# Performance work log

Measured on AMD Instinct MI355X. Metric: run time of the kernel, lower is better.

The kernel has to match this reference:

```python
import jax, jax.numpy as jnp
import numpy as np

N, E, H, C, HC = 16384, 262144, 4, 128, 512
G, IN, ED, OUT, NCLS = 8, 5, 2, 256, 12
EPS = 1e-5


def _gatv2(x, src, dst, ea, Wl, Wr, We, att, b):
    # GATv2Conv (PyG): score = att . leaky_relu(lin_l(x_j) + lin_r(x_i) + lin_e(e))
    xl = (x @ Wl).reshape(-1, H, C)          # source transform [N,H,C]
    xr = (x @ Wr).reshape(-1, H, C)          # target transform [N,H,C]
    ee = (ea @ We).reshape(-1, H, C)         # edge embedding   [E,H,C]
    s = jax.nn.leaky_relu(xl[src] + xr[dst] + ee, 0.2)
    logit = jnp.einsum('ehc,hc->eh', s, att)            # [E,H]
    m = jax.ops.segment_max(logit, dst, num_segments=N)  # per-dst max
    a = jnp.exp(logit - m[dst])
    denom = jax.ops.segment_sum(a, dst, num_segments=N)
    alpha = a / (denom[dst] + 1e-16)                     # segment softmax
    out = jax.ops.segment_sum(xl[src] * alpha[:, :, None], dst, num_segments=N)
    return out.reshape(-1, HC) + b


def _bn(x, g, b):  # BatchNorm1d, training-mode batch stats
    mu = x.mean(0)
    var = x.var(0)
    return g * (x - mu) * jax.lax.rsqrt(var + EPS) + b


def setup_inputs() -> dict:
    key = jax.random.key(0)
    ks = iter(jax.random.split(key, 32))
    d = {}
    d['x'] = jax.random.normal(next(ks), (N, IN), jnp.float32)
    d['edge_attr'] = jax.random.normal(next(ks), (E, ED), jnp.float32)
    d['edge_index'] = jax.random.randint(next(ks), (2, E), 0, N)
    d['batch'] = jnp.sort(jax.random.randint(next(ks), (N,), 0, G))
    for i, din in zip((1, 2, 3), (IN, HC, HC)):
        d[f'c{i}_Wl'] = jax.random.normal(next(ks), (din, HC), jnp.float32) * 0.05
        d[f'c{i}_Wr'] = jax.random.normal(next(ks), (din, HC), jnp.float32) * 0.05
        d[f'c{i}_We'] = jax.random.normal(next(ks), (ED, HC), jnp.float32) * 0.05
        d[f'c{i}_att'] = jax.random.normal(next(ks), (H, C), jnp.float32) * 0.05
        d[f'c{i}_b'] = jnp.zeros((HC,), jnp.float32)
        d[f'bn{i}_g'] = jnp.ones((HC,), jnp.float32)
        d[f'bn{i}_b'] = jnp.zeros((HC,), jnp.float32)
    d['ge_W1'] = jax.random.normal(next(ks), (HC, OUT), jnp.float32) * 0.05
    d['ge_b1'] = jnp.zeros((OUT,), jnp.float32)
    d['ge_W2'] = jax.random.normal(next(ks), (OUT, OUT), jnp.float32) * 0.05
    d['ge_b2'] = jnp.zeros((OUT,), jnp.float32)
    d['cls_W'] = jax.random.normal(next(ks), (OUT, NCLS), jnp.float32) * 0.05
    d['cls_b'] = jnp.zeros((NCLS,), jnp.float32)
    return d


def reference(x, edge_attr, edge_index, batch,
              c1_Wl, c1_Wr, c1_We, c1_att, c1_b, bn1_g, bn1_b,
              c2_Wl, c2_Wr, c2_We, c2_att, c2_b, bn2_g, bn2_b,
              c3_Wl, c3_Wr, c3_We, c3_att, c3_b, bn3_g, bn3_b,
              ge_W1, ge_b1, ge_W2, ge_b2, cls_W, cls_b):
    src, dst = edge_index[0], edge_index[1]
    x1 = jax.nn.elu(_bn(_gatv2(x, src, dst, edge_attr, c1_Wl, c1_Wr, c1_We, c1_att, c1_b), bn1_g, bn1_b))
    x2 = jax.nn.elu(_bn(_gatv2(x1, src, dst, edge_attr, c2_Wl, c2_Wr, c2_We, c2_att, c2_b), bn2_g, bn2_b)) + x1
    x3 = jax.nn.elu(_bn(_gatv2(x2, src, dst, edge_attr, c3_Wl, c3_Wr, c3_We, c3_att, c3_b), bn3_g, bn3_b)) + x2
    cnt = jax.ops.segment_sum(jnp.ones((N,), x3.dtype), batch, num_segments=G)
    x_pool = jax.ops.segment_sum(x3, batch, num_segments=G) / cnt[:, None]
    emb = jax.nn.relu(x_pool @ ge_W1 + ge_b1) @ ge_W2 + ge_b2
    logits = emb @ cls_W + cls_b
    return logits, emb
```

## Files before the change

### kernel.cpp

```cpp
#include <hip/hip_runtime.h>
#include <math.h>

#define NN    16384
#define NE    262144
#define NHEAD 4
#define HC    512
#define NG    8

typedef __bf16 bf16x8 __attribute__((ext_vector_type(8)));
typedef float floatx4 __attribute__((ext_vector_type(4)));
typedef float f32x2 __attribute__((ext_vector_type(2)));

__device__ __forceinline__ f32x2 sp2(float s) { return (f32x2){s, s}; }
__device__ __forceinline__ f32x2 pkmax(f32x2 a, f32x2 b) {
    f32x2 r; r.x = fmaxf(a.x, b.x); r.y = fmaxf(a.y, b.y); return r;
}

__device__ __forceinline__ unsigned short f2bf(float f) {
    union { float f; unsigned u; } v{f};
    unsigned r = v.u + 0x7FFFu + ((v.u >> 16) & 1u);
    return (unsigned short)(r >> 16);
}
__device__ __forceinline__ float bf2f(unsigned short b) {
    return __uint_as_float((unsigned)b << 16);
}

__device__ __forceinline__ void unpk8v(uint4 v, f32x2* f) {
    f[0] = (f32x2){__uint_as_float(v.x << 16), __uint_as_float(v.x & 0xFFFF0000u)};
    f[1] = (f32x2){__uint_as_float(v.y << 16), __uint_as_float(v.y & 0xFFFF0000u)};
    f[2] = (f32x2){__uint_as_float(v.z << 16), __uint_as_float(v.z & 0xFFFF0000u)};
    f[3] = (f32x2){__uint_as_float(v.w << 16), __uint_as_float(v.w & 0xFFFF0000u)};
}

#define GLD16(g, l) __builtin_amdgcn_global_load_lds( \
    (const __attribute__((address_space(1))) void*)(g), \
    (__attribute__((address_space(3))) void*)(l), 16, 0, 0)

__global__ void k_hist(const int* __restrict__ dst, int* __restrict__ cnt) {
    int e = blockIdx.x * 256 + threadIdx.x;
    if (e < NE) atomicAdd(&cnt[dst[e]], 1);
}

__global__ __launch_bounds__(1024) void k_scan(const int* __restrict__ cnt,
                                               int* __restrict__ rp,
                                               int* __restrict__ offp,
                                               const int* __restrict__ batch,
                                               int* __restrict__ gcnt) {
    __shared__ int part[1024];
    int t = threadIdx.x;
    if (t < NG) {
        int lb[2];
#pragma unroll
        for (int q = 0; q < 2; q++) {
            int target = t + q;
            int lo = 0, hi = NN;
            while (lo < hi) {
                int mid = (lo + hi) >> 1;
                if (batch[mid] < target) lo = mid + 1; else hi = mid;
            }
            lb[q] = lo;
        }
        gcnt[t] = lb[1] - lb[0];
    }
    int base = t * 16;
    int loc[16];
    int s = 0;
#pragma unroll
    for (int i = 0; i < 16; i++) { loc[i] = s; s += cnt[base + i]; }
    part[t] = s;
    __syncthreads();
    for (int off = 1; off < 1024; off <<= 1) {
        int v = 0;
        if (t >= off) v = part[t - off];
        __syncthreads();
        if (t >= off) part[t] += v;
        __syncthreads();
    }
    int excl = (t == 0) ? 0 : part[t - 1];
#pragma unroll
    for (int i = 0; i < 16; i++) {
        int r = excl + loc[i];
        rp[base + i] = r;
        offp[base + i] = r;
    }
    if (t == 1023) rp[NN] = excl + s;
}

__global__ void k_fill(const int* __restrict__ dst, const int* __restrict__ src,
                       const float* __restrict__ ea, int* __restrict__ offp,
                       int* __restrict__ csrc, float2* __restrict__ ce) {
    int e = blockIdx.x * 256 + threadIdx.x;
    if (e < NE) {
        int d = dst[e];
        int pos = atomicAdd(&offp[d], 1);
        csrc[pos] = src[e];
        ce[pos] = *(const float2*)(ea + 2 * (size_t)e);
    }
}

__global__ __launch_bounds__(256) void k_lin1(const float* __restrict__ x,
                                              const float* __restrict__ Wl,
                                              const float* __restrict__ Wr,
                                              unsigned short* __restrict__ xl,
                                              unsigned short* __restrict__ xr) {
    int n = blockIdx.x * 4 + (threadIdx.x >> 6);
    int lane = threadIdx.x & 63;
    int j0 = lane << 3;
    float xs[5];
#pragma unroll
    for (int k = 0; k < 5; k++) xs[k] = x[n * 5 + k];
    float al[8] = {}, ar[8] = {};
#pragma unroll
    for (int k = 0; k < 5; k++) {
        float4 wl0 = *(const float4*)(Wl + k * 512 + j0);
        float4 wl1 = *(const float4*)(Wl + k * 512 + j0 + 4);
        float4 wr0 = *(const float4*)(Wr + k * 512 + j0);
        float4 wr1 = *(const float4*)(Wr + k * 512 + j0 + 4);
        al[0] += xs[k] * wl0.x; al[1] += xs[k] * wl0.y; al[2] += xs[k] * wl0.z; al[3] += xs[k] * wl0.w;
        al[4] += xs[k] * wl1.x; al[5] += xs[k] * wl1.y; al[6] += xs[k] * wl1.z; al[7] += xs[k] * wl1.w;
        ar[0] += xs[k] * wr0.x; ar[1] += xs[k] * wr0.y; ar[2] += xs[k] * wr0.z; ar[3] += xs[k] * wr0.w;
        ar[4] += xs[k] * wr1.x; ar[5] += xs[k] * wr1.y; ar[6] += xs[k] * wr1.z; ar[7] += xs[k] * wr1.w;
    }
    ushort4 o0, o1;
    o0.x = f2bf(al[0]); o0.y = f2bf(al[1]); o0.z = f2bf(al[2]); o0.w = f2bf(al[3]);
    o1.x = f2bf(al[4]); o1.y = f2bf(al[5]); o1.z = f2bf(al[6]); o1.w = f2bf(al[7]);
    *(ushort4*)(xl + (size_t)n * 512 + j0) = o0;
    *(ushort4*)(xl + (size_t)n * 512 + j0 + 4) = o1;
    o0.x = f2bf(ar[0]); o0.y = f2bf(ar[1]); o0.z = f2bf(ar[2]); o0.w = f2bf(ar[3]);
    o1.x = f2bf(ar[4]); o1.y = f2bf(ar[5]); o1.z = f2bf(ar[6]); o1.w = f2bf(ar[7]);
    *(ushort4*)(xr + (size_t)n * 512 + j0) = o0;
    *(ushort4*)(xr + (size_t)n * 512 + j0 + 4) = o1;
}

__global__ __launch_bounds__(256) void k_wt4(const float* __restrict__ W0,
                                             const float* __restrict__ W1,
                                             const float* __restrict__ W2,
                                             const float* __restrict__ W3,
                                             unsigned short* __restrict__ Wt2,
                                             unsigned short* __restrict__ Wt3) {
    __shared__ float tile[64][65];
    int bid = blockIdx.x;
    int mat = bid >> 6, sub = bid & 63;
    const float* W = (mat == 0) ? W0 : (mat == 1) ? W1 : (mat == 2) ? W2 : W3;
    unsigned short* Wt = (mat == 0) ? Wt2 : (mat == 1) ? (Wt2 + 512 * 512)
                       : (mat == 2) ? Wt3 : (Wt3 + 512 * 512);
    int n0 = (sub & 7) * 64, k0 = (sub >> 3) * 64;
    int lr = threadIdx.x >> 4;
    int lc = (threadIdx.x & 15) << 2;
    for (int r = lr; r < 64; r += 16) {
        float4 v = *(const float4*)(W + (size_t)(k0 + r) * 512 + n0 + lc);
        tile[r][lc] = v.x; tile[r][lc + 1] = v.y; tile[r][lc + 2] = v.z; tile[r][lc + 3] = v.w;
    }
    __syncthreads();
    for (int r = lr; r < 64; r += 16) {
        ushort4 o;
        o.x = f2bf(tile[lc + 0][r]); o.y = f2bf(tile[lc + 1][r]);
        o.z = f2bf(tile[lc + 2][r]); o.w = f2bf(tile[lc + 3][r]);
        *(ushort4*)(Wt + (size_t)(n0 + r) * 512 + k0 + lc) = o;
    }
}

#define BM 128
#define BN 128
#define BK 64

__global__ __launch_bounds__(256) void k_gemm_bf16(
        const unsigned short* __restrict__ Ab,
        const unsigned short* __restrict__ Bt,
        unsigned short* __restrict__ xl, unsigned short* __restrict__ xr) {
    __shared__ unsigned short As[BM * BK];
    __shared__ unsigned short Bs[BN * BK];
    int t = threadIdx.x;
    int bid = blockIdx.x;
    int xcd = bid & 7, r = bid >> 3;
    int m0 = (xcd * 16 + (r & 15)) * BM;
    int n0 = (r >> 4) * BN;
    int wid = t >> 6, lane = t & 63;
    int wm = (wid >> 1) * 64, wn = (wid & 1) * 64;
    int lrow = lane & 15, quad = lane >> 4;
    floatx4 acc[4][4] = {};
    for (int k0 = 0; k0 < 512; k0 += BK) {
        __syncthreads();
#pragma unroll
        for (int it = 0; it < 4; it++) {
            int cid = it * 256 + t;
            int row = cid >> 3, ch = cid & 7;
            GLD16(Ab + (size_t)(m0 + row) * 512 + k0 + ch * 8, As + cid * 8);
            GLD16(Bt + (size_t)(n0 + row) * 512 + k0 + ch * 8, Bs + cid * 8);
        }
        __syncthreads();
#pragma unroll
        for (int ko = 0; ko < 2; ko++) {
            bf16x8 af[4], bfr[4];
#pragma unroll
            for (int i = 0; i < 4; i++) {
                af[i]  = *(const bf16x8*)&As[(wm + i * 16 + lrow) * BK + ko * 32 + quad * 8];
                bfr[i] = *(const bf16x8*)&Bs[(wn + i * 16 + lrow) * BK + ko * 32 + quad * 8];
            }
#pragma unroll
            for (int i = 0; i < 4; i++)
#pragma unroll
                for (int j = 0; j < 4; j++)
                    acc[i][j] = __builtin_amdgcn_mfma_f32_16x16x32_bf16(af[i], bfr[j], acc[i][j], 0, 0, 0);
        }
    }
#pragma unroll
    for (int i = 0; i < 4; i++) {
        int row = m0 + wm + i * 16 + quad * 4;
#pragma unroll
        for (int j = 0; j < 4; j++) {
            int col = n0 + wn + j * 16 + lrow;
            unsigned short* dstp = (col < 512) ? (xl + (size_t)row * 512 + col)
                                               : (xr + (size_t)row * 512 + (col - 512));
#pragma unroll
            for (int rr = 0; rr < 4; rr++) dstp[(size_t)rr * 512] = f2bf(acc[i][j][rr]);
        }
    }
}

__global__ __launch_bounds__(256) void k_attn(
        const unsigned short* __restrict__ xl, const unsigned short* __restrict__ xr,
        const int* __restrict__ rp, const int* __restrict__ csrc,
        const float2* __restrict__ ce, const float* __restrict__ We,
        const float* __restrict__ att, const float* __restrict__ bias,
        unsigned short* __restrict__ out) {
    int n = __builtin_amdgcn_readfirstlane(blockIdx.x * 4 + (threadIdx.x >> 6));
    int lane = threadIdx.x & 63;
    int c0 = lane << 3;
    f32x2 wv0[4], wv1[4], av[4], rv[4];
    {
        float4 a = *(const float4*)(We + c0), b = *(const float4*)(We + c0 + 4);
        wv0[0] = (f32x2){a.x, a.y}; wv0[1] = (f32x2){a.z, a.w};
        wv0[2] = (f32x2){b.x, b.y}; wv0[3] = (f32x2){b.z, b.w};
        a = *(const float4*)(We + 512 + c0); b = *(const float4*)(We + 512 + c0 + 4);
        wv1[0] = (f32x2){a.x, a.y}; wv1[1] = (f32x2){a.z, a.w};
        wv1[2] = (f32x2){b.x, b.y}; wv1[3] = (f32x2){b.z, b.w};
        a = *(const float4*)(att + c0); b = *(const float4*)(att + c0 + 4);
        av[0] = (f32x2){a.x, a.y}; av[1] = (f32x2){a.z, a.w};
        av[2] = (f32x2){b.x, b.y}; av[3] = (f32x2){b.z, b.w};
        uint4 vr = *(const uint4*)(xr + (size_t)n * 512 + c0);
        unpk8v(vr, rv);
    }
    float l = 0.f;
    f32x2 acc[4] = {sp2(0.f), sp2(0.f), sp2(0.f), sp2(0.f)};
    int beg = rp[n], end = rp[n + 1];
    uint4 cv[4];
    float2 cev[4];
    if (beg < end) {
#pragma unroll
        for (int k = 0; k < 4; k++) {
            int q = beg + k; q = (q < end) ? q : end - 1;
            cv[k] = *(const uint4*)(xl + (size_t)csrc[q] * 512 + c0);
            cev[k] = ce[q];
        }
    }
    int i = beg;
    for (; i + 3 < end; i += 4) {
        uint4 a[4]; float2 d[4];
#pragma unroll
        for (int k = 0; k < 4; k++) { a[k] = cv[k]; d[k] = cev[k]; }
#pragma unroll
        for (int k = 0; k < 4; k++) {
            int q = i + 4 + k; q = (q < end) ? q : end - 1;
            cv[k] = *(const uint4*)(xl + (size_t)csrc[q] * 512 + c0);
            cev[k] = ce[q];
        }
        f32x2 lv[4][4];
#pragma unroll
        for (int k = 0; k < 4; k++) unpk8v(a[k], lv[k]);
        float p[4];
#pragma unroll
        for (int k = 0; k < 4; k++) {
            f32x2 dx = sp2(d[k].x), dy = sp2(d[k].y);
            f32x2 pv = sp2(0.f);
#pragma unroll
            for (int j = 0; j < 4; j++) {
                f32x2 v = lv[k][j] + rv[j] + dx * wv0[j] + dy * wv1[j];
                v = pkmax(v, sp2(0.2f) * v);
                pv += av[j] * v;
            }
            p[k] = pv.x + pv.y;
        }
#pragma unroll
        for (int m = 1; m <= 8; m <<= 1) {
#pragma unroll
            for (int k = 0; k < 4; k++) p[k] += __shfl_xor(p[k], m);
        }
        float w[4];
#pragma unroll
        for (int k = 0; k < 4; k++) { w[k] = __expf(fminf(p[k], 60.f)); l += w[k]; }
#pragma unroll
        for (int j = 0; j < 4; j++) {
            f32x2 t0 = sp2(w[0]) * lv[0][j] + sp2(w[1]) * lv[1][j];
            f32x2 t1 = sp2(w[2]) * lv[2][j] + sp2(w[3]) * lv[3][j];
            acc[j] += t0 + t1;
        }
    }
    int rem = end - i;
#pragma unroll
    for (int k = 0; k < 3; k++) {
        if (k < rem) {
            f32x2 lv[4];
            unpk8v(cv[k], lv);
            f32x2 dx = sp2(cev[k].x), dy = sp2(cev[k].y);
            f32x2 pv = sp2(0.f);
#pragma unroll
            for (int j = 0; j < 4; j++) {
                f32x2 v = lv[j] + rv[j] + dx * wv0[j] + dy * wv1[j];
                v = pkmax(v, sp2(0.2f) * v);
                pv += av[j] * v;
            }
            float p = pv.x + pv.y;
            p += __shfl_xor(p, 1);
            p += __shfl_xor(p, 2);
            p += __shfl_xor(p, 4);
            p += __shfl_xor(p, 8);
            float w = __expf(fminf(p, 60.f));
            l += w;
            f32x2 wv = sp2(w);
#pragma unroll
            for (int j = 0; j < 4; j++) acc[j] += wv * lv[j];
        }
    }
    float inv = 1.f / (l + 1e-16f);
    const float* bb = bias + c0;
    float4 b0 = *(const float4*)bb, b1 = *(const float4*)(bb + 4);
    ushort4 o0, o1;
    o0.x = f2bf(acc[0].x * inv + b0.x); o0.y = f2bf(acc[0].y * inv + b0.y);
    o0.z = f2bf(acc[1].x * inv + b0.z); o0.w = f2bf(acc[1].y * inv + b0.w);
    o1.x = f2bf(acc[2].x * inv + b1.x); o1.y = f2bf(acc[2].y * inv + b1.y);
    o1.z = f2bf(acc[3].x * inv + b1.z); o1.w = f2bf(acc[3].y * inv + b1.w);
    *(ushort4*)(out + (size_t)n * 512 + c0) = o0;
    *(ushort4*)(out + (size_t)n * 512 + c0 + 4) = o1;
}

__global__ __launch_bounds__(256) void k_bnstat(const unsigned short* __restrict__ xb,
                                                double* __restrict__ sum,
                                                double* __restrict__ sumsq) {
    int t = threadIdx.x;
    int r0 = blockIdx.x * 64;
    int c2 = t << 1;
    float s0 = 0.f, s1 = 0.f, q0 = 0.f, q1 = 0.f;
    for (int r = r0; r < r0 + 64; r++) {
        unsigned u = *(const unsigned*)(xb + (size_t)r * 512 + c2);
        float v0 = __uint_as_float(u << 16);
        float v1 = __uint_as_float(u & 0xFFFF0000u);
        s0 += v0; q0 += v0 * v0;
        s1 += v1; q1 += v1 * v1;
    }
    atomicAdd(sum + c2, (double)s0);
    atomicAdd(sum + c2 + 1, (double)s1);
    atomicAdd(sumsq + c2, (double)q0);
    atomicAdd(sumsq + c2 + 1, (double)q1);
}

__global__ void k_bnapply(const unsigned short* __restrict__ v,
                          const unsigned short* __restrict__ resid,
                          const double* __restrict__ sum, const double* __restrict__ sumsq,
                          const float* __restrict__ g, const float* __restrict__ beta,
                          unsigned short* __restrict__ outb) {
    int i = (blockIdx.x * 256 + threadIdx.x) << 2;
    int c = i & 511;
    ushort4 vu = *(const ushort4*)(v + i);
    double2 s01 = *(const double2*)(sum + c);
    double2 s23 = *(const double2*)(sum + c + 2);
    double2 q01 = *(const double2*)(sumsq + c);
    double2 q23 = *(const double2*)(sumsq + c + 2);
    float4 gg = *(const float4*)(g + c);
    float4 be = *(const float4*)(beta + c);
    const double invN = 1.0 / NN;
    double mu0 = s01.x * invN, mu1 = s01.y * invN, mu2 = s23.x * invN, mu3 = s23.y * invN;
    float sc0 = gg.x * rsqrtf((float)(q01.x * invN - mu0 * mu0) + 1e-5f);
    float sc1 = gg.y * rsqrtf((float)(q01.y * invN - mu1 * mu1) + 1e-5f);
    float sc2 = gg.z * rsqrtf((float)(q23.x * invN - mu2 * mu2) + 1e-5f);
    float sc3 = gg.w * rsqrtf((float)(q23.y * invN - mu3 * mu3) + 1e-5f);
    float y0 = (bf2f(vu.x) - (float)mu0) * sc0 + be.x;
    float y1 = (bf2f(vu.y) - (float)mu1) * sc1 + be.y;
    float y2 = (bf2f(vu.z) - (float)mu2) * sc2 + be.z;
    float y3 = (bf2f(vu.w) - (float)mu3) * sc3 + be.w;
    y0 = y0 > 0.f ? y0 : expm1f(y0);
    y1 = y1 > 0.f ? y1 : expm1f(y1);
    y2 = y2 > 0.f ? y2 : expm1f(y2);
    y3 = y3 > 0.f ? y3 : expm1f(y3);
    if (resid) {
        ushort4 ru = *(const ushort4*)(resid + i);
        y0 += bf2f(ru.x); y1 += bf2f(ru.y); y2 += bf2f(ru.z); y3 += bf2f(ru.w);
    }
    ushort4 o;
    o.x = f2bf(y0); o.y = f2bf(y1); o.z = f2bf(y2); o.w = f2bf(y3);
    *(ushort4*)(outb + i) = o;
}

__global__ __launch_bounds__(256) void k_pool(const unsigned short* __restrict__ xb,
                                              const int* __restrict__ batch,
                                              float* __restrict__ pooled) {
    __shared__ float lacc[NG][512];
    int t = threadIdx.x;
    for (int i = t; i < NG * 512; i += 256) ((float*)lacc)[i] = 0.f;
    __syncthreads();
    int r0 = blockIdx.x * 64;
    int c2 = t << 1;
    for (int r = r0; r < r0 + 64; r++) {
        int g = batch[r];
        unsigned u = *(const unsigned*)(xb + (size_t)r * 512 + c2);
        lacc[g][c2]     += __uint_as_float(u << 16);
        lacc[g][c2 + 1] += __uint_as_float(u & 0xFFFF0000u);
    }
    __syncthreads();
    int gmin = batch[r0], gmax = batch[r0 + 63];
    for (int g = gmin; g <= gmax; g++)
        for (int i = t; i < 512; i += 256)
            atomicAdd(&pooled[g * 512 + i], lacc[g][i]);
}

__global__ __launch_bounds__(256) void k_head_h1(const float* __restrict__ pooled,
                                                 const float* __restrict__ W1,
                                                 float* __restrict__ h1acc) {
    int g = blockIdx.x >> 4, s = blockIdx.x & 15;
    int o = threadIdx.x;
    int c0 = s * 32;
    float acc = 0.f;
#pragma unroll
    for (int c = 0; c < 32; c++)
        acc += pooled[g * 512 + c0 + c] * W1[(size_t)(c0 + c) * 256 + o];
    atomicAdd(&h1acc[g * 256 + o], acc);
}

__global__ __launch_bounds__(256) void k_head_emb(const float* __restrict__ h1acc,
                                                  const int* __restrict__ gcnt,
                                                  const float* __restrict__ b1,
                                                  const float* __restrict__ W2,
                                                  float* __restrict__ embacc) {
    __shared__ float hs[32];
    int g = blockIdx.x >> 3, s = blockIdx.x & 7;
    int c0 = s * 32;
    int t = threadIdx.x;
    if (t < 32) {
        float inv = 1.f / (float)gcnt[g];
        hs[t] = fmaxf(h1acc[g * 256 + c0 + t] * inv + b1[c0 + t], 0.f);
    }
    __syncthreads();
    float acc = 0.f;
#pragma unroll
    for (int c = 0; c < 32; c++)
        acc += hs[c] * W2[(size_t)(c0 + c) * 256 + t];
    atomicAdd(&embacc[g * 256 + t], acc);
}

__global__ __launch_bounds__(256) void k_head_fin(const float* __restrict__ embacc,
                                                  const float* __restrict__ b2,
                                                  const float* __restrict__ clsW,
                                                  const float* __restrict__ clsb,
                                                  float* __restrict__ outp) {
    __shared__ float es[256];
    int g = blockIdx.x, o = threadIdx.x;
    float e = embacc[g * 256 + o] + b2[o];
    outp[NG * 12 + g * 256 + o] = e;
    es[o] = e;
    __syncthreads();
    if (o < 12) {
        float lg = clsb[o];
        for (int c = 0; c < 256; c++) lg += es[c] * clsW[c * 12 + o];
        outp[g * 12 + o] = lg;
    }
}

extern "C" void kernel_launch(void* const* d_in, const int* in_sizes, int n_in,
                              void* d_out, int out_size, void* d_ws, size_t ws_size,
                              hipStream_t stream) {
    const float* x     = (const float*)d_in[0];
    const float* ea    = (const float*)d_in[1];
    const int*   ei    = (const int*)d_in[2];
    const int*   batch = (const int*)d_in[3];
    const int* src = ei;
    const int* dst = ei + NE;

    float* base = (float*)d_ws;
    size_t off = 0;
    auto alloc = [&](size_t n) -> float* {
        float* p = base + off;
        off += (n + 255) & ~(size_t)255;
        return p;
    };
    unsigned short* xl  = (unsigned short*)alloc((size_t)NN * 256);
    unsigned short* xr  = (unsigned short*)alloc((size_t)NN * 256);
    unsigned short* Yb  = (unsigned short*)alloc((size_t)NN * 256);
    unsigned short* XbA = (unsigned short*)alloc((size_t)NN * 256);
    unsigned short* XbB = (unsigned short*)alloc((size_t)NN * 256);
    unsigned short* Wt2 = (unsigned short*)alloc(512 * 1024 / 2);
    unsigned short* Wt3 = (unsigned short*)alloc(512 * 1024 / 2);
    int*      rp    = (int*)alloc(NN + 1);
    int*      offp  = (int*)alloc(NN);
    int*      csrc  = (int*)alloc(NE);
    float2*   ce    = (float2*)alloc((size_t)NE * 2);
    int*      cnt   = (int*)alloc(NN);
    double*   bsum3 = (double*)alloc(3 * 2048);
    float*    pooled= alloc(NG * 512);
    float*    h1acc = alloc(NG * 256);
    float*    embacc= alloc(NG * 256);
    int*      gcnt  = (int*)alloc(NG);
    float*    outp  = (float*)d_out;

    hipMemsetAsync(cnt, 0, 30720 * sizeof(float), stream);
    k_hist<<<NE / 256, 256, 0, stream>>>(dst, cnt);
    k_scan<<<1, 1024, 0, stream>>>(cnt, rp, offp, batch, gcnt);
    k_fill<<<NE / 256, 256, 0, stream>>>(dst, src, ea, offp, csrc, ce);
    k_wt4<<<256, 256, 0, stream>>>((const float*)d_in[11], (const float*)d_in[12],
                                   (const float*)d_in[18], (const float*)d_in[19], Wt2, Wt3);

    unsigned short* X = XbA;
    unsigned short* Xp = XbB;
    for (int l = 0; l < 3; l++) {
        const float* Wl  = (const float*)d_in[4 + l * 7 + 0];
        const float* Wr  = (const float*)d_in[4 + l * 7 + 1];
        const float* We  = (const float*)d_in[4 + l * 7 + 2];
        const float* att = (const float*)d_in[4 + l * 7 + 3];
        const float* cb  = (const float*)d_in[4 + l * 7 + 4];
        const float* bg  = (const float*)d_in[4 + l * 7 + 5];
        const float* bb  = (const float*)d_in[4 + l * 7 + 6];

        if (l == 0) {
            k_lin1<<<NN / 4, 256, 0, stream>>>(x, Wl, Wr, xl, xr);
        } else {
            k_gemm_bf16<<<1024, 256, 0, stream>>>(Xp, (l == 1) ? Wt2 : Wt3, xl, xr);
        }
        k_attn<<<NN / 4, 256, 0, stream>>>(xl, xr, rp, csrc, ce, We, att, cb, Yb);

        double* bsum = bsum3 + l * 1024;
        double* bsq  = bsum + 512;
        k_bnstat<<<256, 256, 0, stream>>>(Yb, bsum, bsq);
        k_bnapply<<<(size_t)NN * 512 / 1024, 256, 0, stream>>>(
            Yb, (l == 0) ? nullptr : Xp, bsum, bsq, bg, bb, X);

        unsigned short* tmp = Xp; Xp = X; X = tmp;
    }

    k_pool<<<NN / 64, 256, 0, stream>>>(Xp, batch, pooled);

    const float* geW1 = (const float*)d_in[25];
    const float* geb1 = (const float*)d_in[26];
    const float* geW2 = (const float*)d_in[27];
    const float* geb2 = (const float*)d_in[28];
    const float* clsW = (const float*)d_in[29];
    const float* clsb = (const float*)d_in[30];

    k_head_h1<<<NG * 16, 256, 0, stream>>>(pooled, geW1, h1acc);
    k_head_emb<<<NG * 8, 256, 0, stream>>>(h1acc, gcnt, geb1, geW2, embacc);
    k_head_fin<<<NG, 256, 0, stream>>>(embacc, geb2, clsW, clsb, outp);
}
```

Baseline: 471.2 us.

## Merge setup kernels, deepen attention gather prefetch, fuse pooling into batchnorm apply

Histogram, weight transpose and first-layer linear are merged into one launch that dispatches on block index. The attention kernel now prefetches neighbor indices two groups ahead and ping-pongs two register buffers so the gathers overlap more with compute. The last layer's batchnorm-apply also does the mean pooling from fp32 values, which removes the separate pool kernel and one re-read of activations. The cost is higher register pressure in attention and a block-size change in bnapply. Pooling now sums unrounded fp32 values, so results may differ slightly from before.

```diff
diff --git a/kernel.cpp b/kernel.cpp
--- a/kernel.cpp
+++ b/kernel.cpp
@@ -35,11 +35,6 @@
 #define GLD16(g, l) __builtin_amdgcn_global_load_lds( \
     (const __attribute__((address_space(1))) void*)(g), \
     (__attribute__((address_space(3))) void*)(l), 16, 0, 0)
-
-__global__ void k_hist(const int* __restrict__ dst, int* __restrict__ cnt) {
-    int e = blockIdx.x * 256 + threadIdx.x;
-    if (e < NE) atomicAdd(&cnt[dst[e]], 1);
-}
 
 __global__ __launch_bounds__(1024) void k_scan(const int* __restrict__ cnt,
                                                int* __restrict__ rp,
@@ -98,65 +93,68 @@
     }
 }
 
-__global__ __launch_bounds__(256) void k_lin1(const float* __restrict__ x,
-                                              const float* __restrict__ Wl,
-                                              const float* __restrict__ Wr,
-                                              unsigned short* __restrict__ xl,
-                                              unsigned short* __restrict__ xr) {
-    int n = blockIdx.x * 4 + (threadIdx.x >> 6);
-    int lane = threadIdx.x & 63;
-    int j0 = lane << 3;
-    float xs[5];
-#pragma unroll
-    for (int k = 0; k < 5; k++) xs[k] = x[n * 5 + k];
-    float al[8] = {}, ar[8] = {};
-#pragma unroll
-    for (int k = 0; k < 5; k++) {
-        float4 wl0 = *(const float4*)(Wl + k * 512 + j0);
-        float4 wl1 = *(const float4*)(Wl + k * 512 + j0 + 4);
-        float4 wr0 = *(const float4*)(Wr + k * 512 + j0);
-        float4 wr1 = *(const float4*)(Wr + k * 512 + j0 + 4);
-        al[0] += xs[k] * wl0.x; al[1] += xs[k] * wl0.y; al[2] += xs[k] * wl0.z; al[3] += xs[k] * wl0.w;
-        al[4] += xs[k] * wl1.x; al[5] += xs[k] * wl1.y; al[6] += xs[k] * wl1.z; al[7] += xs[k] * wl1.w;
-        ar[0] += xs[k] * wr0.x; ar[1] += xs[k] * wr0.y; ar[2] += xs[k] * wr0.z; ar[3] += xs[k] * wr0.w;
-        ar[4] += xs[k] * wr1.x; ar[5] += xs[k] * wr1.y; ar[6] += xs[k] * wr1.z; ar[7] += xs[k] * wr1.w;
-    }
-    ushort4 o0, o1;
-    o0.x = f2bf(al[0]); o0.y = f2bf(al[1]); o0.z = f2bf(al[2]); o0.w = f2bf(al[3]);
-    o1.x = f2bf(al[4]); o1.y = f2bf(al[5]); o1.z = f2bf(al[6]); o1.w = f2bf(al[7]);
-    *(ushort4*)(xl + (size_t)n * 512 + j0) = o0;
-    *(ushort4*)(xl + (size_t)n * 512 + j0 + 4) = o1;
-    o0.x = f2bf(ar[0]); o0.y = f2bf(ar[1]); o0.z = f2bf(ar[2]); o0.w = f2bf(ar[3]);
-    o1.x = f2bf(ar[4]); o1.y = f2bf(ar[5]); o1.z = f2bf(ar[6]); o1.w = f2bf(ar[7]);
-    *(ushort4*)(xr + (size_t)n * 512 + j0) = o0;
-    *(ushort4*)(xr + (size_t)n * 512 + j0 + 4) = o1;
-}
-
-__global__ __launch_bounds__(256) void k_wt4(const float* __restrict__ W0,
-                                             const float* __restrict__ W1,
-                                             const float* __restrict__ W2,
-                                             const float* __restrict__ W3,
-                                             unsigned short* __restrict__ Wt2,
-                                             unsigned short* __restrict__ Wt3) {
+__global__ __launch_bounds__(256) void k_pre(
+        const int* __restrict__ dst, int* __restrict__ cnt,
+        const float* __restrict__ W0, const float* __restrict__ W1,
+        const float* __restrict__ W2, const float* __restrict__ W3,
+        unsigned short* __restrict__ Wt2, unsigned short* __restrict__ Wt3,
+        const float* __restrict__ x, const float* __restrict__ Wl,
+        const float* __restrict__ Wr,
+        unsigned short* __restrict__ xl, unsigned short* __restrict__ xr) {
     __shared__ float tile[64][65];
     int bid = blockIdx.x;
-    int mat = bid >> 6, sub = bid & 63;
-    const float* W = (mat == 0) ? W0 : (mat == 1) ? W1 : (mat == 2) ? W2 : W3;
-    unsigned short* Wt = (mat == 0) ? Wt2 : (mat == 1) ? (Wt2 + 512 * 512)
-                       : (mat == 2) ? Wt3 : (Wt3 + 512 * 512);
-    int n0 = (sub & 7) * 64, k0 = (sub >> 3) * 64;
-    int lr = threadIdx.x >> 4;
-    int lc = (threadIdx.x & 15) << 2;
-    for (int r = lr; r < 64; r += 16) {
-        float4 v = *(const float4*)(W + (size_t)(k0 + r) * 512 + n0 + lc);
-        tile[r][lc] = v.x; tile[r][lc + 1] = v.y; tile[r][lc + 2] = v.z; tile[r][lc + 3] = v.w;
-    }
-    __syncthreads();
-    for (int r = lr; r < 64; r += 16) {
-        ushort4 o;
-        o.x = f2bf(tile[lc + 0][r]); o.y = f2bf(tile[lc + 1][r]);
-        o.z = f2bf(tile[lc + 2][r]); o.w = f2bf(tile[lc + 3][r]);
-        *(ushort4*)(Wt + (size_t)(n0 + r) * 512 + k0 + lc) = o;
+    int t = threadIdx.x;
+    if (bid >= 1280) {
+        int n = (bid - 1280) * 4 + (t >> 6);
+        int lane = t & 63;
+        int j0 = lane << 3;
+        float xs[5];
+#pragma unroll
+        for (int k = 0; k < 5; k++) xs[k] = x[n * 5 + k];
+        float al[8] = {}, ar[8] = {};
+#pragma unroll
+        for (int k = 0; k < 5; k++) {
+            float4 wl0 = *(const float4*)(Wl + k * 512 + j0);
+            float4 wl1 = *(const float4*)(Wl + k * 512 + j0 + 4);
+            float4 wr0 = *(const float4*)(Wr + k * 512 + j0);
+            float4 wr1 = *(const float4*)(Wr + k * 512 + j0 + 4);
+            al[0] += xs[k] * wl0.x; al[1] += xs[k] * wl0.y; al[2] += xs[k] * wl0.z; al[3] += xs[k] * wl0.w;
+            al[4] += xs[k] * wl1.x; al[5] += xs[k] * wl1.y; al[6] += xs[k] * wl1.z; al[7] += xs[k] * wl1.w;
+            ar[0] += xs[k] * wr0.x; ar[1] += xs[k] * wr0.y; ar[2] += xs[k] * wr0.z; ar[3] += xs[k] * wr0.w;
+            ar[4] += xs[k] * wr1.x; ar[5] += xs[k] * wr1.y; ar[6] += xs[k] * wr1.z; ar[7] += xs[k] * wr1.w;
+        }
+        ushort4 o0, o1;
+        o0.x = f2bf(al[0]); o0.y = f2bf(al[1]); o0.z = f2bf(al[2]); o0.w = f2bf(al[3]);
+        o1.x = f2bf(al[4]); o1.y = f2bf(al[5]); o1.z = f2bf(al[6]); o1.w = f2bf(al[7]);
+        *(ushort4*)(xl + (size_t)n * 512 + j0) = o0;
+        *(ushort4*)(xl + (size_t)n * 512 + j0 + 4) = o1;
+        o0.x = f2bf(ar[0]); o0.y = f2bf(ar[1]); o0.z = f2bf(ar[2]); o0.w = f2bf(ar[3]);
+        o1.x = f2bf(ar[4]); o1.y = f2bf(ar[5]); o1.z = f2bf(ar[6]); o1.w = f2bf(ar[7]);
+        *(ushort4*)(xr + (size_t)n * 512 + j0) = o0;
+        *(ushort4*)(xr + (size_t)n * 512 + j0 + 4) = o1;
+    } else if (bid >= 1024) {
+        int wb = bid - 1024;
+        int mat = wb >> 6, sub = wb & 63;
+        const float* W = (mat == 0) ? W0 : (mat == 1) ? W1 : (mat == 2) ? W2 : W3;
+        unsigned short* Wt = (mat == 0) ? Wt2 : (mat == 1) ? (Wt2 + 512 * 512)
+                           : (mat == 2) ? Wt3 : (Wt3 + 512 * 512);
+        int n0 = (sub & 7) * 64, k0 = (sub >> 3) * 64;
+        int lr = t >> 4;
+        int lc = (t & 15) << 2;
+        for (int r = lr; r < 64; r += 16) {
+            float4 v = *(const float4*)(W + (size_t)(k0 + r) * 512 + n0 + lc);
+            tile[r][lc] = v.x; tile[r][lc + 1] = v.y; tile[r][lc + 2] = v.z; tile[r][lc + 3] = v.w;
+        }
+        __syncthreads();
+        for (int r = lr; r < 64; r += 16) {
+            ushort4 o;
+            o.x = f2bf(tile[lc + 0][r]); o.y = f2bf(tile[lc + 1][r]);
+            o.z = f2bf(tile[lc + 2][r]); o.w = f2bf(tile[lc + 3][r]);
+            *(ushort4*)(Wt + (size_t)(n0 + r) * 512 + k0 + lc) = o;
+        }
+    } else {
+        int e = bid * 256 + t;
+        atomicAdd(&cnt[dst[e]], 1);
     }
 }
 
@@ -217,6 +215,54 @@
         }
     }
 }
+
+#define COMPUTE4(CV, CE) do { \
+    f32x2 lv[4][4]; \
+    _Pragma("unroll") for (int k = 0; k < 4; k++) unpk8v(CV[k], lv[k]); \
+    float p[4]; \
+    _Pragma("unroll") for (int k = 0; k < 4; k++) { \
+        f32x2 dx = sp2(CE[k].x), dy = sp2(CE[k].y); \
+        f32x2 pv = sp2(0.f); \
+        _Pragma("unroll") for (int j = 0; j < 4; j++) { \
+            f32x2 vv = lv[k][j] + rv[j] + dx * wv0[j] + dy * wv1[j]; \
+            vv = pkmax(vv, sp2(0.2f) * vv); \
+            pv += av[j] * vv; \
+        } \
+        p[k] = pv.x + pv.y; \
+    } \
+    _Pragma("unroll") for (int m = 1; m <= 8; m <<= 1) { \
+        _Pragma("unroll") for (int k = 0; k < 4; k++) p[k] += __shfl_xor(p[k], m); \
+    } \
+    float w[4]; \
+    _Pragma("unroll") for (int k = 0; k < 4; k++) { w[k] = __expf(fminf(p[k], 60.f)); l += w[k]; } \
+    _Pragma("unroll") for (int j = 0; j < 4; j++) { \
+        f32x2 t0 = sp2(w[0]) * lv[0][j] + sp2(w[1]) * lv[1][j]; \
+        f32x2 t1 = sp2(w[2]) * lv[2][j] + sp2(w[3]) * lv[3][j]; \
+        acc[j] += t0 + t1; \
+    } \
+} while (0)
+
+#define ATTN_TAIL(CV, CE) do { \
+    _Pragma("unroll") for (int k = 0; k < 3; k++) { \
+        if (k < rem) { \
+            f32x2 lv[4]; unpk8v(CV[k], lv); \
+            f32x2 dx = sp2(CE[k].x), dy = sp2(CE[k].y); \
+            f32x2 pv = sp2(0.f); \
+            _Pragma("unroll") for (int j = 0; j < 4; j++) { \
+                f32x2 vv = lv[j] + rv[j] + dx * wv0[j] + dy * wv1[j]; \
+                vv = pkmax(vv, sp2(0.2f) * vv); \
+                pv += av[j] * vv; \
+            } \
+            float p = pv.x + pv.y; \
+            p += __shfl_xor(p, 1); p += __shfl_xor(p, 2); \
+            p += __shfl_xor(p, 4); p += __shfl_xor(p, 8); \
+            float w = __expf(fminf(p, 60.f)); \
+            l += w; \
+            f32x2 wvv = sp2(w); \
+            _Pragma("unroll") for (int j = 0; j < 4; j++) acc[j] += wvv * lv[j]; \
+        } \
+    } \
+} while (0)
 
 __global__ __launch_bounds__(256) void k_attn(
         const unsigned short* __restrict__ xl, const unsigned short* __restrict__ xr,
@@ -244,83 +290,58 @@
     float l = 0.f;
     f32x2 acc[4] = {sp2(0.f), sp2(0.f), sp2(0.f), sp2(0.f)};
     int beg = rp[n], end = rp[n + 1];
-    uint4 cv[4];
-    float2 cev[4];
+    uint4 cvA[4], cvB[4];
+    float2 ceA[4], ceB[4];
+    int idx[4];
+    float2 cpf[4];
     if (beg < end) {
 #pragma unroll
         for (int k = 0; k < 4; k++) {
             int q = beg + k; q = (q < end) ? q : end - 1;
-            cv[k] = *(const uint4*)(xl + (size_t)csrc[q] * 512 + c0);
-            cev[k] = ce[q];
+            cvA[k] = *(const uint4*)(xl + (size_t)csrc[q] * 512 + c0);
+            ceA[k] = ce[q];
+        }
+#pragma unroll
+        for (int k = 0; k < 4; k++) {
+            int q = beg + 4 + k; q = (q < end) ? q : end - 1;
+            idx[k] = csrc[q];
+            cpf[k] = ce[q];
         }
     }
     int i = beg;
+    int useA = 1;
     for (; i + 3 < end; i += 4) {
-        uint4 a[4]; float2 d[4];
-#pragma unroll
-        for (int k = 0; k < 4; k++) { a[k] = cv[k]; d[k] = cev[k]; }
-#pragma unroll
-        for (int k = 0; k < 4; k++) {
-            int q = i + 4 + k; q = (q < end) ? q : end - 1;
-            cv[k] = *(const uint4*)(xl + (size_t)csrc[q] * 512 + c0);
-            cev[k] = ce[q];
-        }
-        f32x2 lv[4][4];
-#pragma unroll
-        for (int k = 0; k < 4; k++) unpk8v(a[k], lv[k]);
-        float p[4];
-#pragma unroll
-        for (int k = 0; k < 4; k++) {
-            f32x2 dx = sp2(d[k].x), dy = sp2(d[k].y);
-            f32x2 pv = sp2(0.f);
-#pragma unroll
-            for (int j = 0; j < 4; j++) {
-                f32x2 v = lv[k][j] + rv[j] + dx * wv0[j] + dy * wv1[j];
-                v = pkmax(v, sp2(0.2f) * v);
-                pv += av[j] * v;
+        if (useA) {
+#pragma unroll
+            for (int k = 0; k < 4; k++) {
+                cvB[k] = *(const uint4*)(xl + (size_t)idx[k] * 512 + c0);
+                ceB[k] = cpf[k];
             }
-            p[k] = pv.x + pv.y;
-        }
-#pragma unroll
-        for (int m = 1; m <= 8; m <<= 1) {
-#pragma unroll
-            for (int k = 0; k < 4; k++) p[k] += __shfl_xor(p[k], m);
-        }
-        float w[4];
-#pragma unroll
-        for (int k = 0; k < 4; k++) { w[k] = __expf(fminf(p[k], 60.f)); l += w[k]; }
-#pragma unroll
-        for (int j = 0; j < 4; j++) {
-            f32x2 t0 = sp2(w[0]) * lv[0][j] + sp2(w[1]) * lv[1][j];
-            f32x2 t1 = sp2(w[2]) * lv[2][j] + sp2(w[3]) * lv[3][j];
-            acc[j] += t0 + t1;
-        }
+#pragma unroll
+            for (int k = 0; k < 4; k++) {
+                int q = i + 8 + k; q = (q < end) ? q : end - 1;
+                idx[k] = csrc[q]; cpf[k] = ce[q];
+            }
+            COMPUTE4(cvA, ceA);
+        } else {
+#pragma unroll
+            for (int k = 0; k < 4; k++) {
+                cvA[k] = *(const uint4*)(xl + (size_t)idx[k] * 512 + c0);
+                ceA[k] = cpf[k];
+            }
+#pragma unroll
+            for (int k = 0; k < 4; k++) {
+                int q = i + 8 + k; q = (q < end) ? q : end - 1;
+                idx[k] = csrc[q]; cpf[k] = ce[q];
+            }
+            COMPUTE4(cvB, ceB);
+        }
+        useA ^= 1;
     }
     int rem = end - i;
-#pragma unroll
-    for (int k = 0; k < 3; k++) {
-        if (k < rem) {
-            f32x2 lv[4];
-            unpk8v(cv[k], lv);
-            f32x2 dx = sp2(cev[k].x), dy = sp2(cev[k].y);
-            f32x2 pv = sp2(0.f);
-#pragma unroll
-            for (int j = 0; j < 4; j++) {
-                f32x2 v = lv[j] + rv[j] + dx * wv0[j] + dy * wv1[j];
-                v = pkmax(v, sp2(0.2f) * v);
-                pv += av[j] * v;
-            }
-            float p = pv.x + pv.y;
-            p += __shfl_xor(p, 1);
-            p += __shfl_xor(p, 2);
-            p += __shfl_xor(p, 4);
-            p += __shfl_xor(p, 8);
-            float w = __expf(fminf(p, 60.f));
-            l += w;
-            f32x2 wv = sp2(w);
-#pragma unroll
-            for (int j = 0; j < 4; j++) acc[j] += wv * lv[j];
-        }
+    if (rem > 0) {
+        if (useA) ATTN_TAIL(cvA, ceA);
+        else      ATTN_TAIL(cvB, ceB);
     }
     float inv = 1.f / (l + 1e-16f);
     const float* bb = bias + c0;
@@ -354,63 +375,59 @@
     atomicAdd(sumsq + c2 + 1, (double)q1);
 }
 
-__global__ void k_bnapply(const unsigned short* __restrict__ v,
-                          const unsigned short* __restrict__ resid,
-                          const double* __restrict__ sum, const double* __restrict__ sumsq,
-                          const float* __restrict__ g, const float* __restrict__ beta,
-                          unsigned short* __restrict__ outb) {
-    int i = (blockIdx.x * 256 + threadIdx.x) << 2;
-    int c = i & 511;
-    ushort4 vu = *(const ushort4*)(v + i);
-    double2 s01 = *(const double2*)(sum + c);
-    double2 s23 = *(const double2*)(sum + c + 2);
-    double2 q01 = *(const double2*)(sumsq + c);
-    double2 q23 = *(const double2*)(sumsq + c + 2);
-    float4 gg = *(const float4*)(g + c);
-    float4 be = *(const float4*)(beta + c);
+__global__ __launch_bounds__(256) void k_bnapply(
+        const unsigned short* __restrict__ v,
+        const unsigned short* __restrict__ resid,
+        const double* __restrict__ sum, const double* __restrict__ sumsq,
+        const float* __restrict__ g, const float* __restrict__ beta,
+        unsigned short* __restrict__ outb,
+        const int* __restrict__ batch,
+        float* __restrict__ pooled) {
+    __shared__ float lacc[NG][512];
+    int t = threadIdx.x;
+    int r0 = blockIdx.x * 64;
+    int c2 = t << 1;
+    double2 s01 = *(const double2*)(sum + c2);
+    double2 q01 = *(const double2*)(sumsq + c2);
+    float2 gg = *(const float2*)(g + c2);
+    float2 be = *(const float2*)(beta + c2);
     const double invN = 1.0 / NN;
-    double mu0 = s01.x * invN, mu1 = s01.y * invN, mu2 = s23.x * invN, mu3 = s23.y * invN;
+    double mu0 = s01.x * invN, mu1 = s01.y * invN;
     float sc0 = gg.x * rsqrtf((float)(q01.x * invN - mu0 * mu0) + 1e-5f);
     float sc1 = gg.y * rsqrtf((float)(q01.y * invN - mu1 * mu1) + 1e-5f);
-    float sc2 = gg.z * rsqrtf((float)(q23.x * invN - mu2 * mu2) + 1e-5f);
-    float sc3 = gg.w * rsqrtf((float)(q23.y * invN - mu3 * mu3) + 1e-5f);
-    float y0 = (bf2f(vu.x) - (float)mu0) * sc0 + be.x;
-    float y1 = (bf2f(vu.y) - (float)mu1) * sc1 + be.y;
-    float y2 = (bf2f(vu.z) - (float)mu2) * sc2 + be.z;
-    float y3 = (bf2f(vu.w) - (float)mu3) * sc3 + be.w;
-    y0 = y0 > 0.f ? y0 : expm1f(y0);
-    y1 = y1 > 0.f ? y1 : expm1f(y1);
-    y2 = y2 > 0.f ? y2 : expm1f(y2);
-    y3 = y3 > 0.f ? y3 : expm1f(y3);
-    if (resid) {
-        ushort4 ru = *(const ushort4*)(resid + i);
-        y0 += bf2f(ru.x); y1 += bf2f(ru.y); y2 += bf2f(ru.z); y3 += bf2f(ru.w);
-    }
-    ushort4 o;
-    o.x = f2bf(y0); o.y = f2bf(y1); o.z = f2bf(y2); o.w = f2bf(y3);
-    *(ushort4*)(outb + i) = o;
-}
-
-__global__ __launch_bounds__(256) void k_pool(const unsigned short* __restrict__ xb,
-                                              const int* __restrict__ batch,
-                                              float* __restrict__ pooled) {
-    __shared__ float lacc[NG][512];
-    int t = threadIdx.x;
-    for (int i = t; i < NG * 512; i += 256) ((float*)lacc)[i] = 0.f;
-    __syncthreads();
-    int r0 = blockIdx.x * 64;
-    int c2 = t << 1;
+    float fm0 = (float)mu0, fm1 = (float)mu1;
+    bool dopool = (batch != nullptr);
+    if (dopool) {
+        for (int i2 = t; i2 < NG * 512; i2 += 256) ((float*)lacc)[i2] = 0.f;
+        __syncthreads();
+    }
+#pragma unroll 4
     for (int r = r0; r < r0 + 64; r++) {
-        int g = batch[r];
-        unsigned u = *(const unsigned*)(xb + (size_t)r * 512 + c2);
-        lacc[g][c2]     += __uint_as_float(u << 16);
-        lacc[g][c2 + 1] += __uint_as_float(u & 0xFFFF0000u);
-    }
-    __syncthreads();
-    int gmin = batch[r0], gmax = batch[r0 + 63];
-    for (int g = gmin; g <= gmax; g++)
-        for (int i = t; i < 512; i += 256)
-            atomicAdd(&pooled[g * 512 + i], lacc[g][i]);
+        unsigned u = *(const unsigned*)(v + (size_t)r * 512 + c2);
+        float y0 = (__uint_as_float(u << 16) - fm0) * sc0 + be.x;
+        float y1 = (__uint_as_float(u & 0xFFFF0000u) - fm1) * sc1 + be.y;
+        y0 = y0 > 0.f ? y0 : expm1f(y0);
+        y1 = y1 > 0.f ? y1 : expm1f(y1);
+        if (resid) {
+            unsigned ru = *(const unsigned*)(resid + (size_t)r * 512 + c2);
+            y0 += __uint_as_float(ru << 16);
+            y1 += __uint_as_float(ru & 0xFFFF0000u);
+        }
+        unsigned o = ((unsigned)f2bf(y0)) | ((unsigned)f2bf(y1) << 16);
+        *(unsigned*)(outb + (size_t)r * 512 + c2) = o;
+        if (dopool) {
+            int gb = batch[r];
+            lacc[gb][c2]     += y0;
+            lacc[gb][c2 + 1] += y1;
+        }
+    }
+    if (dopool) {
+        __syncthreads();
+        int gmin = batch[r0], gmax = batch[r0 + 63];
+        for (int gb = gmin; gb <= gmax; gb++)
+            for (int i2 = t; i2 < 512; i2 += 256)
+                atomicAdd(&pooled[gb * 512 + i2], lacc[gb][i2]);
+    }
 }
 
 __global__ __launch_bounds__(256) void k_head_h1(const float* __restrict__ pooled,
@@ -502,26 +519,25 @@
     float*    outp  = (float*)d_out;
 
     hipMemsetAsync(cnt, 0, 30720 * sizeof(float), stream);
-    k_hist<<<NE / 256, 256, 0, stream>>>(dst, cnt);
+    k_pre<<<5376, 256, 0, stream>>>(dst, cnt,
+                                    (const float*)d_in[11], (const float*)d_in[12],
+                                    (const float*)d_in[18], (const float*)d_in[19],
+                                    Wt2, Wt3,
+                                    x, (const float*)d_in[4], (const float*)d_in[5],
+                                    xl, xr);
     k_scan<<<1, 1024, 0, stream>>>(cnt, rp, offp, batch, gcnt);
     k_fill<<<NE / 256, 256, 0, stream>>>(dst, src, ea, offp, csrc, ce);
-    k_wt4<<<256, 256, 0, stream>>>((const float*)d_in[11], (const float*)d_in[12],
-                                   (const float*)d_in[18], (const float*)d_in[19], Wt2, Wt3);
 
     unsigned short* X = XbA;
     unsigned short* Xp = XbB;
     for (int l = 0; l < 3; l++) {
-        const float* Wl  = (const float*)d_in[4 + l * 7 + 0];
-        const float* Wr  = (const float*)d_in[4 + l * 7 + 1];
         const float* We  = (const float*)d_in[4 + l * 7 + 2];
         const float* att = (const float*)d_in[4 + l * 7 + 3];
         const float* cb  = (const float*)d_in[4 + l * 7 + 4];
         const float* bg  = (const float*)d_in[4 + l * 7 + 5];
         const float* bb  = (const float*)d_in[4 + l * 7 + 6];
 
-        if (l == 0) {
-            k_lin1<<<NN / 4, 256, 0, stream>>>(x, Wl, Wr, xl, xr);
-        } else {
+        if (l > 0) {
             k_gemm_bf16<<<1024, 256, 0, stream>>>(Xp, (l == 1) ? Wt2 : Wt3, xl, xr);
         }
         k_attn<<<NN / 4, 256, 0, stream>>>(xl, xr, rp, csrc, ce, We, att, cb, Yb);
@@ -529,13 +545,12 @@
         double* bsum = bsum3 + l * 1024;
         double* bsq  = bsum + 512;
         k_bnstat<<<256, 256, 0, stream>>>(Yb, bsum, bsq);
-        k_bnapply<<<(size_t)NN * 512 / 1024, 256, 0, stream>>>(
-            Yb, (l == 0) ? nullptr : Xp, bsum, bsq, bg, bb, X);
+        k_bnapply<<<NN / 64, 256, 0, stream>>>(
+            Yb, (l == 0) ? nullptr : Xp, bsum, bsq, bg, bb, X,
+            (l == 2) ? batch : nullptr, pooled);
 
         unsigned short* tmp = Xp; Xp = X; X = tmp;
     }
-
-    k_pool<<<NN / 64, 256, 0, stream>>>(Xp, batch, pooled);
 
     const float* geW1 = (const float*)d_in[25];
     const float* geb1 = (const float*)d_in[26];
```

Result: slower. 540.0 us (+14.6%).
